# Kernel optimization log

Measured on AMD Instinct MI355X. Metric: run time of the kernel, lower is better.

Reference implementation:

```python
import jax, jax.numpy as jnp
import numpy as np


def _grid_sample_2d(plane, gx, gy):
    """Bilinear sample plane (C,H,W) at normalized coords gx,gy in [-1,1].
    align_corners=True convention (standard in tri-plane NeRF code).
    Returns (N, C)."""
    C, H, W = plane.shape
    ix = (gx + 1.0) * 0.5 * (W - 1)  # x indexes width
    iy = (gy + 1.0) * 0.5 * (H - 1)  # y indexes height
    x0f = jnp.floor(ix)
    y0f = jnp.floor(iy)
    wx = ix - x0f  # (N,)
    wy = iy - y0f
    x0 = jnp.clip(x0f.astype(jnp.int32), 0, W - 1)
    x1 = jnp.clip(x0 + 1, 0, W - 1)
    y0 = jnp.clip(y0f.astype(jnp.int32), 0, H - 1)
    y1 = jnp.clip(y0 + 1, 0, H - 1)
    flat = plane.reshape(C, H * W)

    def gather(yi, xi):  # -> (N, C)
        return jnp.take(flat, yi * W + xi, axis=1).T

    w00 = ((1 - wx) * (1 - wy))[:, None]
    w01 = (wx * (1 - wy))[:, None]
    w10 = ((1 - wx) * wy)[:, None]
    w11 = (wx * wy)[:, None]
    return (gather(y0, x0) * w00 + gather(y0, x1) * w01 +
            gather(y1, x0) * w10 + gather(y1, x1) * w11)


def setup_inputs() -> dict:
    key = jax.random.key(0)
    ks = jax.random.split(key, 7)
    N, C, H1, H2 = 2097152, 32, 256, 4
    res = (727, 314, 1300)
    pts = jax.random.uniform(ks[0], (N, 3), jnp.float32, minval=-1.0, maxval=1.0)
    s = 0.1  # small init like typical plane init
    plane_yx = jax.random.normal(ks[1], (C, res[1], res[0]), jnp.float32) * s
    plane_zx = jax.random.normal(ks[2], (C, res[2], res[0]), jnp.float32) * s
    plane_zy = jax.random.normal(ks[3], (C, res[2], res[1]), jnp.float32) * s
    w1 = jax.random.normal(ks[4], (C, H1), jnp.float32) * (1.0 / np.sqrt(C))
    b1 = jnp.zeros((H1,), jnp.float32)
    w2 = jax.random.normal(ks[5], (H1, H2), jnp.float32) * (1.0 / np.sqrt(H1))
    b2 = jnp.zeros((H2,), jnp.float32)
    return {"pts": pts, "plane_yx": plane_yx, "plane_zx": plane_zx,
            "plane_zy": plane_zy, "w1": w1, "b1": b1, "w2": w2, "b2": b2}


def reference(pts, plane_yx, plane_zx, plane_zy, w1, b1, w2, b2):
    # tri-plane feature fetch: pairs (x,y), (x,z), (y,z)
    f_yx = _grid_sample_2d(plane_yx, pts[:, 0], pts[:, 1])  # (N, C)
    f_zx = _grid_sample_2d(plane_zx, pts[:, 0], pts[:, 2])
    f_zy = _grid_sample_2d(plane_zy, pts[:, 1], pts[:, 2])
    features = f_yx * f_zx * f_zy  # elementwise product over planes
    h = jax.nn.relu(features @ w1 + b1)  # decoder MLP
    out = h @ w2 + b2  # (N, out_dim)
    return out
```

## Files before the change

kernel.cpp:

```cpp
#include <hip/hip_runtime.h>

#define NC    32
#define NH1   256
#define W_YX  727
#define H_YX  314
#define W_ZX  727
#define H_ZX  1300
#define W_ZY  314
#define H_ZY  1300
#define HW_YX (W_YX * H_YX)
#define HW_ZX (W_ZX * H_ZX)
#define HW_ZY (W_ZY * H_ZY)

#define FSTRIDE 17

typedef __attribute__((ext_vector_type(8))) short short8;
typedef __attribute__((ext_vector_type(4))) float f32x4;

__device__ __forceinline__ short f2bf(float f) {
    unsigned u = __float_as_uint(f);
    unsigned r = u + 0x7fffu + ((u >> 16) & 1u);
    return (short)(r >> 16);
}

__global__ __launch_bounds__(256) void kplane_transpose_bf16(
    const float* __restrict__ src, unsigned short* __restrict__ dst, int HW)
{
    __shared__ float tile[32][129];
    int hw0 = blockIdx.x * 128;
    int tx = threadIdx.x & 31, ty = threadIdx.x >> 5;
    if (hw0 + 128 <= HW) {
#pragma unroll
        for (int i = 0; i < 4; ++i) {
            int c = ty + i * 8;
            float4 v = *(const float4*)(src + (size_t)c * HW + hw0 + tx * 4);
            tile[c][tx * 4 + 0] = v.x; tile[c][tx * 4 + 1] = v.y;
            tile[c][tx * 4 + 2] = v.z; tile[c][tx * 4 + 3] = v.w;
        }
    } else {
        for (int i = 0; i < 4; ++i) {
            int c = ty + i * 8;
            for (int e = 0; e < 4; ++e) {
                int hw = hw0 + tx * 4 + e;
                tile[c][tx * 4 + e] = (hw < HW) ? src[(size_t)c * HW + hw] : 0.0f;
            }
        }
    }
    __syncthreads();
    int c8 = threadIdx.x & 3, r0 = threadIdx.x >> 2;
#pragma unroll
    for (int i = 0; i < 2; ++i) {
        int r = r0 + i * 64;
        int hw = hw0 + r;
        if (hw < HW) {
            uint4 o;
            unsigned* ou = (unsigned*)&o;
#pragma unroll
            for (int e = 0; e < 4; ++e) {
                unsigned lo = (unsigned)(unsigned short)f2bf(tile[c8 * 8 + 2 * e][r]);
                unsigned hi = (unsigned)(unsigned short)f2bf(tile[c8 * 8 + 2 * e + 1][r]);
                ou[e] = lo | (hi << 16);
            }
            *(uint4*)(dst + (size_t)hw * NC + c8 * 8) = o;
        }
    }
}

__global__ __launch_bounds__(256) void kplane_prep_w1(
    const float* __restrict__ w1, short* __restrict__ wb)
{
    int idx = blockIdx.x * 256 + threadIdx.x;
    int jj   = idx & 7;
    int lane = (idx >> 3) & 63;
    int nt   = idx >> 9;
    int n = nt * 16 + (lane & 15);
    int k = (lane >> 4) * 8 + jj;
    wb[idx] = f2bf(w1[k * NH1 + n]);
}

__device__ __forceinline__ void bilin2(
    float gx, float gy, int W, int H,
    unsigned& o0, unsigned& o1, float& wx, float& wy)
{
    float ix  = (gx + 1.0f) * 0.5f * (float)(W - 1);
    float iy  = (gy + 1.0f) * 0.5f * (float)(H - 1);
    float x0f = floorf(ix), y0f = floorf(iy);
    wx = ix - x0f; wy = iy - y0f;
    int x0 = (int)x0f; x0 = x0 < 0 ? 0 : (x0 > W - 1 ? W - 1 : x0);
    int y0 = (int)y0f; y0 = y0 < 0 ? 0 : (y0 > H - 1 ? H - 1 : y0);
    int y1 = y0 + 1; if (y1 > H - 1) y1 = H - 1;
    o0 = (unsigned)(y0 * W + x0) * 64u;
    o1 = (unsigned)(y1 * W + x0) * 64u;
}

__device__ __forceinline__ void sample8(
    const unsigned short* __restrict__ plane,
    unsigned o0, unsigned o1, float wy, float wxv, int j, float F[8])
{
    uint4 u0 = *(const uint4*)((const char*)plane + (size_t)o0 + j * 16);
    uint4 u1 = *(const uint4*)((const char*)plane + (size_t)o1 + j * 16);
    unsigned ua[4] = {u0.x, u0.y, u0.z, u0.w};
    unsigned ub[4] = {u1.x, u1.y, u1.z, u1.w};
#pragma unroll
    for (int e = 0; e < 4; ++e) {
        float a0 = __uint_as_float(ua[e] << 16);
        float a1 = __uint_as_float(ua[e] & 0xffff0000u);
        float b0 = __uint_as_float(ub[e] << 16);
        float b1 = __uint_as_float(ub[e] & 0xffff0000u);
        F[2 * e]     = wxv * fmaf(wy, b0 - a0, a0);
        F[2 * e + 1] = wxv * fmaf(wy, b1 - a1, a1);
    }
#pragma unroll
    for (int e = 0; e < 8; ++e)
        F[e] += __shfl_xor(F[e], 4, 64);
}

__global__ __launch_bounds__(256) void kplane_fused(
    const float* __restrict__ pts,
    const unsigned short* __restrict__ tyx,
    const unsigned short* __restrict__ tzx,
    const unsigned short* __restrict__ tzy,
    const short* __restrict__ w1b,
    const float* __restrict__ b1, const float* __restrict__ w2,
    const float* __restrict__ b2,
    float* __restrict__ out)
{
    __shared__ unsigned featS[256 * FSTRIDE];

    int t = threadIdx.x;
    int base = blockIdx.x * 256;
    int l = t & 63, j = t & 7;

    float px = pts[(size_t)(base + t) * 3 + 0];
    float py = pts[(size_t)(base + t) * 3 + 1];
    float pz = pts[(size_t)(base + t) * 3 + 2];
    unsigned ao0, ao1, co0, co1, do0, do1;
    float awx, awy, cwx, cwy, dwx, dwy;
    bilin2(px, py, W_YX, H_YX, ao0, ao1, awx, awy);
    bilin2(px, pz, W_ZX, H_ZX, co0, co1, cwx, cwy);
    bilin2(py, pz, W_ZY, H_ZY, do0, do1, dwx, dwy);

#pragma unroll
    for (int r = 0; r < 8; ++r) {
        int srcl = (l & 0x38) | r;
        int p = (t & ~7) | r;

        unsigned A0 = (unsigned)__shfl((int)ao0, srcl, 64);
        unsigned A1 = (unsigned)__shfl((int)ao1, srcl, 64);
        float AX = __shfl(awx, srcl, 64), AY = __shfl(awy, srcl, 64);
        unsigned C0 = (unsigned)__shfl((int)co0, srcl, 64);
        unsigned C1 = (unsigned)__shfl((int)co1, srcl, 64);
        float CX = __shfl(cwx, srcl, 64), CY = __shfl(cwy, srcl, 64);
        unsigned D0 = (unsigned)__shfl((int)do0, srcl, 64);
        unsigned D1 = (unsigned)__shfl((int)do1, srcl, 64);
        float DX = __shfl(dwx, srcl, 64), DY = __shfl(dwy, srcl, 64);

        float axv = (j & 4) ? AX : 1.0f - AX;
        float cxv = (j & 4) ? CX : 1.0f - CX;
        float dxv = (j & 4) ? DX : 1.0f - DX;

        float acc[8], tmp[8];
        sample8(tyx, A0, A1, AY, axv, j, acc);
        sample8(tzx, C0, C1, CY, cxv, j, tmp);
#pragma unroll
        for (int e = 0; e < 8; ++e) acc[e] *= tmp[e];
        sample8(tzy, D0, D1, DY, dxv, j, tmp);
#pragma unroll
        for (int e = 0; e < 8; ++e) acc[e] *= tmp[e];

        if (j < 4) {
#pragma unroll
            for (int e = 0; e < 4; ++e) {
                unsigned lo = (unsigned)(unsigned short)f2bf(acc[2 * e]);
                unsigned hi = (unsigned)(unsigned short)f2bf(acc[2 * e + 1]);
                featS[p * FSTRIDE + j * 4 + e] = lo | (hi << 16);
            }
        }
    }
    __syncthreads();

    {
        int w = t >> 6;
        int quad = l >> 4, l15 = l & 15;
        float4 b2v = *(const float4*)b2;
        const short8* Bw = (const short8*)w1b;

#pragma unroll
        for (int mt = 0; mt < 4; ++mt) {
            int p = w * 64 + mt * 16 + l15;
            union { unsigned u[4]; short8 s; } A;
#pragma unroll
            for (int e = 0; e < 4; ++e)
                A.u[e] = featS[p * FSTRIDE + quad * 4 + e];

            float4 oo0 = {0,0,0,0}, oo1 = {0,0,0,0}, oo2 = {0,0,0,0}, oo3 = {0,0,0,0};
#pragma unroll
            for (int nt = 0; nt < 16; ++nt) {
                short8 bh = Bw[nt * 64 + l];
                f32x4 z = {0.f, 0.f, 0.f, 0.f};
                z = __builtin_amdgcn_mfma_f32_16x16x32_bf16(A.s, bh, z, 0, 0, 0);
                float  b1v = b1[nt * 16 + l15];
                float4 w2v = ((const float4*)w2)[nt * 16 + l15];
                float h0 = fmaxf(z[0] + b1v, 0.f);
                float h1 = fmaxf(z[1] + b1v, 0.f);
                float h2 = fmaxf(z[2] + b1v, 0.f);
                float h3 = fmaxf(z[3] + b1v, 0.f);
                oo0.x = fmaf(h0, w2v.x, oo0.x); oo0.y = fmaf(h0, w2v.y, oo0.y);
                oo0.z = fmaf(h0, w2v.z, oo0.z); oo0.w = fmaf(h0, w2v.w, oo0.w);
                oo1.x = fmaf(h1, w2v.x, oo1.x); oo1.y = fmaf(h1, w2v.y, oo1.y);
                oo1.z = fmaf(h1, w2v.z, oo1.z); oo1.w = fmaf(h1, w2v.w, oo1.w);
                oo2.x = fmaf(h2, w2v.x, oo2.x); oo2.y = fmaf(h2, w2v.y, oo2.y);
                oo2.z = fmaf(h2, w2v.z, oo2.z); oo2.w = fmaf(h2, w2v.w, oo2.w);
                oo3.x = fmaf(h3, w2v.x, oo3.x); oo3.y = fmaf(h3, w2v.y, oo3.y);
                oo3.z = fmaf(h3, w2v.z, oo3.z); oo3.w = fmaf(h3, w2v.w, oo3.w);
            }
#pragma unroll
            for (int d = 1; d < 16; d <<= 1) {
                oo0.x += __shfl_xor(oo0.x, d); oo0.y += __shfl_xor(oo0.y, d);
                oo0.z += __shfl_xor(oo0.z, d); oo0.w += __shfl_xor(oo0.w, d);
                oo1.x += __shfl_xor(oo1.x, d); oo1.y += __shfl_xor(oo1.y, d);
                oo1.z += __shfl_xor(oo1.z, d); oo1.w += __shfl_xor(oo1.w, d);
                oo2.x += __shfl_xor(oo2.x, d); oo2.y += __shfl_xor(oo2.y, d);
                oo2.z += __shfl_xor(oo2.z, d); oo2.w += __shfl_xor(oo2.w, d);
                oo3.x += __shfl_xor(oo3.x, d); oo3.y += __shfl_xor(oo3.y, d);
                oo3.z += __shfl_xor(oo3.z, d); oo3.w += __shfl_xor(oo3.w, d);
            }
            if (l15 == 0) {
                int ptg = base + w * 64 + mt * 16 + quad * 4;
                float4* O = (float4*)out;
                float4 r0 = {oo0.x + b2v.x, oo0.y + b2v.y, oo0.z + b2v.z, oo0.w + b2v.w};
                float4 r1 = {oo1.x + b2v.x, oo1.y + b2v.y, oo1.z + b2v.z, oo1.w + b2v.w};
                float4 r2 = {oo2.x + b2v.x, oo2.y + b2v.y, oo2.z + b2v.z, oo2.w + b2v.w};
                float4 r3 = {oo3.x + b2v.x, oo3.y + b2v.y, oo3.z + b2v.z, oo3.w + b2v.w};
                O[ptg + 0] = r0; O[ptg + 1] = r1; O[ptg + 2] = r2; O[ptg + 3] = r3;
            }
        }
    }
}

__device__ __forceinline__ void bilin_full(
    float gx, float gy, int W, int H,
    int& o00, int& o01, int& o10, int& o11,
    float& w00, float& w01, float& w10, float& w11)
{
    float ix  = (gx + 1.0f) * 0.5f * (float)(W - 1);
    float iy  = (gy + 1.0f) * 0.5f * (float)(H - 1);
    float x0f = floorf(ix), y0f = floorf(iy);
    float wx  = ix - x0f,   wy  = iy - y0f;
    int x0 = (int)x0f; x0 = x0 < 0 ? 0 : (x0 > W - 1 ? W - 1 : x0);
    int y0 = (int)y0f; y0 = y0 < 0 ? 0 : (y0 > H - 1 ? H - 1 : y0);
    int x1 = x0 + 1; if (x1 > W - 1) x1 = W - 1;
    int y1 = y0 + 1; if (y1 > H - 1) y1 = H - 1;
    o00 = y0 * W + x0; o01 = y0 * W + x1;
    o10 = y1 * W + x0; o11 = y1 * W + x1;
    w00 = (1.0f - wx) * (1.0f - wy);
    w01 = wx * (1.0f - wy);
    w10 = (1.0f - wx) * wy;
    w11 = wx * wy;
}

__global__ __launch_bounds__(256) void kplane_fused_direct(
    const float* __restrict__ pts,
    const float* __restrict__ pyx, const float* __restrict__ pzx,
    const float* __restrict__ pzy,
    const float* __restrict__ w1, const float* __restrict__ b1,
    const float* __restrict__ w2, const float* __restrict__ b2,
    float* __restrict__ out, int N)
{
    int i = blockIdx.x * blockDim.x + threadIdx.x;
    if (i >= N) return;
    float px = pts[(size_t)i * 3 + 0];
    float py = pts[(size_t)i * 3 + 1];
    float pz = pts[(size_t)i * 3 + 2];

    int a00, a01, a10, a11; float aw00, aw01, aw10, aw11;
    int c00, c01, c10, c11; float cw00, cw01, cw10, cw11;
    int d00, d01, d10, d11; float dw00, dw01, dw10, dw11;
    bilin_full(px, py, W_YX, H_YX, a00, a01, a10, a11, aw00, aw01, aw10, aw11);
    bilin_full(px, pz, W_ZX, H_ZX, c00, c01, c10, c11, cw00, cw01, cw10, cw11);
    bilin_full(py, pz, W_ZY, H_ZY, d00, d01, d10, d11, dw00, dw01, dw10, dw11);

    float feat[NC];
#pragma unroll 4
    for (int c = 0; c < NC; ++c) {
        const float* byx = pyx + (size_t)c * HW_YX;
        const float* bzx = pzx + (size_t)c * HW_ZX;
        const float* bzy = pzy + (size_t)c * HW_ZY;
        float fyx = aw00 * byx[a00] + aw01 * byx[a01] + aw10 * byx[a10] + aw11 * byx[a11];
        float fzx = cw00 * bzx[c00] + cw01 * bzx[c01] + cw10 * bzx[c10] + cw11 * bzx[c11];
        float fzy = dw00 * bzy[d00] + dw01 * bzy[d01] + dw10 * bzy[d10] + dw11 * bzy[d11];
        feat[c] = fyx * fzx * fzy;
    }
    float o0 = b2[0], o1 = b2[1], o2 = b2[2], o3 = b2[3];
#pragma unroll 4
    for (int k = 0; k < NH1; ++k) {
        float hk = b1[k];
#pragma unroll
        for (int c = 0; c < NC; ++c)
            hk = fmaf(feat[c], w1[c * NH1 + k], hk);
        hk = fmaxf(hk, 0.0f);
        o0 = fmaf(hk, w2[k * 4 + 0], o0);
        o1 = fmaf(hk, w2[k * 4 + 1], o1);
        o2 = fmaf(hk, w2[k * 4 + 2], o2);
        o3 = fmaf(hk, w2[k * 4 + 3], o3);
    }
    float4 o; o.x = o0; o.y = o1; o.z = o2; o.w = o3;
    reinterpret_cast<float4*>(out)[i] = o;
}

extern "C" void kernel_launch(void* const* d_in, const int* in_sizes, int n_in,
                              void* d_out, int out_size, void* d_ws, size_t ws_size,
                              hipStream_t stream)
{
    const float* pts = (const float*)d_in[0];
    const float* pyx = (const float*)d_in[1];
    const float* pzx = (const float*)d_in[2];
    const float* pzy = (const float*)d_in[3];
    const float* w1  = (const float*)d_in[4];
    const float* b1  = (const float*)d_in[5];
    const float* w2  = (const float*)d_in[6];
    const float* b2  = (const float*)d_in[7];
    float* out = (float*)d_out;

    int N = in_sizes[0] / 3;

    size_t planes_e = (size_t)(HW_YX + HW_ZX + HW_ZY) * NC;
    size_t need = planes_e * sizeof(short) + 8192 * sizeof(short) + 256;

    if (ws_size >= need && (N % 256) == 0) {
        unsigned short* tyx = (unsigned short*)d_ws;
        unsigned short* tzx = tyx + (size_t)HW_YX * NC;
        unsigned short* tzy = tzx + (size_t)HW_ZX * NC;
        short* w1b = (short*)(tzy + (size_t)HW_ZY * NC);
        kplane_transpose_bf16<<<(HW_YX + 127) / 128, 256, 0, stream>>>(pyx, tyx, HW_YX);
        kplane_transpose_bf16<<<(HW_ZX + 127) / 128, 256, 0, stream>>>(pzx, tzx, HW_ZX);
        kplane_transpose_bf16<<<(HW_ZY + 127) / 128, 256, 0, stream>>>(pzy, tzy, HW_ZY);
        kplane_prep_w1<<<32, 256, 0, stream>>>(w1, w1b);
        kplane_fused<<<N / 256, 256, 0, stream>>>(pts, tyx, tzx, tzy,
                                                  w1b, b1, w2, b2, out);
    } else {
        int blocks = (N + 255) / 256;
        kplane_fused_direct<<<blocks, 256, 0, stream>>>(pts, pyx, pzx, pzy,
                                                        w1, b1, w2, b2, out, N);
    }
}
```

Before: 645.7 us.

## Move second MLP layer onto MFMA and restructure gather to four lanes per point

The second decoder layer, previously per-lane FMAs followed by a shuffle reduction, now runs as a bf16 MFMA. W1 is used as the A operand so the hidden activations come out already in the B-operand layout, and w2 is pre-packed with zero padding into that layout. The gather stage now stages per-point offsets and weights in shared memory and has four lanes per point each fetch 16-byte slices of all four corners, replacing the 8-lane shuffle and xor-reduce scheme. Hidden activations are rounded to bf16 before the second matmul, which adds precision loss, and the layer-2 MFMA pads its output dimension from 4 to 16.

```diff
diff --git a/kernel.cpp b/kernel.cpp
--- a/kernel.cpp
+++ b/kernel.cpp
@@ -1,4 +1,6 @@
 #include <hip/hip_runtime.h>
+#include <hip/hip_fp16.h>
+#include <hip/hip_bf16.h>
 
 #define NC    32
 #define NH1   256
@@ -12,7 +14,8 @@
 #define HW_ZX (W_ZX * H_ZX)
 #define HW_ZY (W_ZY * H_ZY)
 
-#define FSTRIDE 17
+#define PSTRIDE 12
+#define FSTRIDE 20
 
 typedef __attribute__((ext_vector_type(8))) short short8;
 typedef __attribute__((ext_vector_type(4))) float f32x4;
@@ -21,6 +24,11 @@
     unsigned u = __float_as_uint(f);
     unsigned r = u + 0x7fffu + ((u >> 16) & 1u);
     return (short)(r >> 16);
+}
+__device__ __forceinline__ unsigned pk2(float a, float b) {
+    union { __hip_bfloat162 h; unsigned u; } c;
+    c.h = __float22bfloat162_rn(make_float2(a, b));
+    return c.u;
 }
 
 __global__ __launch_bounds__(256) void kplane_transpose_bf16(
@@ -56,29 +64,40 @@
             uint4 o;
             unsigned* ou = (unsigned*)&o;
 #pragma unroll
-            for (int e = 0; e < 4; ++e) {
-                unsigned lo = (unsigned)(unsigned short)f2bf(tile[c8 * 8 + 2 * e][r]);
-                unsigned hi = (unsigned)(unsigned short)f2bf(tile[c8 * 8 + 2 * e + 1][r]);
-                ou[e] = lo | (hi << 16);
-            }
+            for (int e = 0; e < 4; ++e)
+                ou[e] = pk2(tile[c8 * 8 + 2 * e][r], tile[c8 * 8 + 2 * e + 1][r]);
             *(uint4*)(dst + (size_t)hw * NC + c8 * 8) = o;
         }
     }
 }
 
-__global__ __launch_bounds__(256) void kplane_prep_w1(
-    const float* __restrict__ w1, short* __restrict__ wb)
+__global__ __launch_bounds__(256) void kplane_prep_w1a(
+    const float* __restrict__ w1, short* __restrict__ w1a)
 {
     int idx = blockIdx.x * 256 + threadIdx.x;
-    int jj   = idx & 7;
+    int j    = idx & 7;
     int lane = (idx >> 3) & 63;
     int nt   = idx >> 9;
-    int n = nt * 16 + (lane & 15);
-    int k = (lane >> 4) * 8 + jj;
-    wb[idx] = f2bf(w1[k * NH1 + n]);
-}
-
-__device__ __forceinline__ void bilin2(
+    int ch  = (lane >> 4) * 8 + j;
+    int hid = nt * 16 + (lane & 15);
+    w1a[idx] = f2bf(w1[ch * NH1 + hid]);
+}
+
+__global__ __launch_bounds__(256) void kplane_prep_w2a(
+    const float* __restrict__ w2, short* __restrict__ w2a)
+{
+    int idx = blockIdx.x * 256 + threadIdx.x;
+    int j    = idx & 7;
+    int lane = (idx >> 3) & 63;
+    int kk   = idx >> 9;
+    int o    = lane & 15;
+    int quad = lane >> 4;
+    int hid  = (2 * kk + (j >> 2)) * 16 + quad * 4 + (j & 3);
+    float v  = (o < 4) ? w2[hid * 4 + o] : 0.0f;
+    w2a[idx] = f2bf(v);
+}
+
+__device__ __forceinline__ void bilin3(
     float gx, float gy, int W, int H,
     unsigned& o0, unsigned& o1, float& wx, float& wy)
 {
@@ -93,26 +112,34 @@
     o1 = (unsigned)(y1 * W + x0) * 64u;
 }
 
-__device__ __forceinline__ void sample8(
-    const unsigned short* __restrict__ plane,
-    unsigned o0, unsigned o1, float wy, float wxv, int j, float F[8])
-{
-    uint4 u0 = *(const uint4*)((const char*)plane + (size_t)o0 + j * 16);
-    uint4 u1 = *(const uint4*)((const char*)plane + (size_t)o1 + j * 16);
-    unsigned ua[4] = {u0.x, u0.y, u0.z, u0.w};
-    unsigned ub[4] = {u1.x, u1.y, u1.z, u1.w};
+template <bool FIRST>
+__device__ __forceinline__ void corner4(
+    const uint4& A, const uint4& B, const uint4& C, const uint4& D,
+    float wx, float wy, float F[8])
+{
+    float w00 = (1.0f - wx) * (1.0f - wy);
+    float w01 = wx * (1.0f - wy);
+    float w10 = (1.0f - wx) * wy;
+    float w11 = wx * wy;
+    const unsigned* ua = &A.x; const unsigned* ub = &B.x;
+    const unsigned* uc = &C.x; const unsigned* ud = &D.x;
 #pragma unroll
     for (int e = 0; e < 4; ++e) {
         float a0 = __uint_as_float(ua[e] << 16);
         float a1 = __uint_as_float(ua[e] & 0xffff0000u);
         float b0 = __uint_as_float(ub[e] << 16);
         float b1 = __uint_as_float(ub[e] & 0xffff0000u);
-        F[2 * e]     = wxv * fmaf(wy, b0 - a0, a0);
-        F[2 * e + 1] = wxv * fmaf(wy, b1 - a1, a1);
-    }
-#pragma unroll
-    for (int e = 0; e < 8; ++e)
-        F[e] += __shfl_xor(F[e], 4, 64);
+        float c0 = __uint_as_float(uc[e] << 16);
+        float c1 = __uint_as_float(uc[e] & 0xffff0000u);
+        float d0 = __uint_as_float(ud[e] << 16);
+        float d1 = __uint_as_float(ud[e] & 0xffff0000u);
+        float v0 = w00 * a0; v0 = fmaf(w01, b0, v0);
+        v0 = fmaf(w10, c0, v0); v0 = fmaf(w11, d0, v0);
+        float v1 = w00 * a1; v1 = fmaf(w01, b1, v1);
+        v1 = fmaf(w10, c1, v1); v1 = fmaf(w11, d1, v1);
+        if (FIRST) { F[2 * e] = v0; F[2 * e + 1] = v1; }
+        else       { F[2 * e] *= v0; F[2 * e + 1] *= v1; }
+    }
 }
 
 __global__ __launch_bounds__(256) void kplane_fused(
@@ -120,119 +147,111 @@
     const unsigned short* __restrict__ tyx,
     const unsigned short* __restrict__ tzx,
     const unsigned short* __restrict__ tzy,
-    const short* __restrict__ w1b,
-    const float* __restrict__ b1, const float* __restrict__ w2,
-    const float* __restrict__ b2,
+    const short* __restrict__ w1a, const short* __restrict__ w2a,
+    const float* __restrict__ b1, const float* __restrict__ b2,
     float* __restrict__ out)
 {
+    __shared__ unsigned parS[256 * PSTRIDE];
     __shared__ unsigned featS[256 * FSTRIDE];
 
     int t = threadIdx.x;
     int base = blockIdx.x * 256;
-    int l = t & 63, j = t & 7;
-
-    float px = pts[(size_t)(base + t) * 3 + 0];
-    float py = pts[(size_t)(base + t) * 3 + 1];
-    float pz = pts[(size_t)(base + t) * 3 + 2];
-    unsigned ao0, ao1, co0, co1, do0, do1;
-    float awx, awy, cwx, cwy, dwx, dwy;
-    bilin2(px, py, W_YX, H_YX, ao0, ao1, awx, awy);
-    bilin2(px, pz, W_ZX, H_ZX, co0, co1, cwx, cwy);
-    bilin2(py, pz, W_ZY, H_ZY, do0, do1, dwx, dwy);
-
-#pragma unroll
-    for (int r = 0; r < 8; ++r) {
-        int srcl = (l & 0x38) | r;
-        int p = (t & ~7) | r;
-
-        unsigned A0 = (unsigned)__shfl((int)ao0, srcl, 64);
-        unsigned A1 = (unsigned)__shfl((int)ao1, srcl, 64);
-        float AX = __shfl(awx, srcl, 64), AY = __shfl(awy, srcl, 64);
-        unsigned C0 = (unsigned)__shfl((int)co0, srcl, 64);
-        unsigned C1 = (unsigned)__shfl((int)co1, srcl, 64);
-        float CX = __shfl(cwx, srcl, 64), CY = __shfl(cwy, srcl, 64);
-        unsigned D0 = (unsigned)__shfl((int)do0, srcl, 64);
-        unsigned D1 = (unsigned)__shfl((int)do1, srcl, 64);
-        float DX = __shfl(dwx, srcl, 64), DY = __shfl(dwy, srcl, 64);
-
-        float axv = (j & 4) ? AX : 1.0f - AX;
-        float cxv = (j & 4) ? CX : 1.0f - CX;
-        float dxv = (j & 4) ? DX : 1.0f - DX;
-
-        float acc[8], tmp[8];
-        sample8(tyx, A0, A1, AY, axv, j, acc);
-        sample8(tzx, C0, C1, CY, cxv, j, tmp);
-#pragma unroll
-        for (int e = 0; e < 8; ++e) acc[e] *= tmp[e];
-        sample8(tzy, D0, D1, DY, dxv, j, tmp);
-#pragma unroll
-        for (int e = 0; e < 8; ++e) acc[e] *= tmp[e];
-
-        if (j < 4) {
-#pragma unroll
-            for (int e = 0; e < 4; ++e) {
-                unsigned lo = (unsigned)(unsigned short)f2bf(acc[2 * e]);
-                unsigned hi = (unsigned)(unsigned short)f2bf(acc[2 * e + 1]);
-                featS[p * FSTRIDE + j * 4 + e] = lo | (hi << 16);
+
+    {
+        float px = pts[(size_t)(base + t) * 3 + 0];
+        float py = pts[(size_t)(base + t) * 3 + 1];
+        float pz = pts[(size_t)(base + t) * 3 + 2];
+        unsigned a0, a1, c0, c1, d0, d1;
+        float awx, awy, cwx, cwy, dwx, dwy;
+        bilin3(px, py, W_YX, H_YX, a0, a1, awx, awy);
+        bilin3(px, pz, W_ZX, H_ZX, c0, c1, cwx, cwy);
+        bilin3(py, pz, W_ZY, H_ZY, d0, d1, dwx, dwy);
+        uint4* P = (uint4*)&parS[t * PSTRIDE];
+        uint4 P0 = {a0, a1, c0, c1};
+        uint4 P1 = {d0, d1, __float_as_uint(awx), __float_as_uint(awy)};
+        uint4 P2 = {__float_as_uint(cwx), __float_as_uint(cwy),
+                    __float_as_uint(dwx), __float_as_uint(dwy)};
+        P[0] = P0; P[1] = P1; P[2] = P2;
+    }
+    __syncthreads();
+
+    {
+        int q = t >> 2, j = t & 3;
+        int jx16 = j * 16;
+        const char* Byx = (const char*)tyx;
+        const char* Bzx = (const char*)tzx;
+        const char* Bzy = (const char*)tzy;
+#pragma unroll
+        for (int r = 0; r < 4; ++r) {
+            int p = r * 64 + q;
+            const uint4* P = (const uint4*)&parS[p * PSTRIDE];
+            uint4 P0 = P[0], P1 = P[1], P2 = P[2];
+            float awx = __uint_as_float(P1.z), awy = __uint_as_float(P1.w);
+            float cwx = __uint_as_float(P2.x), cwy = __uint_as_float(P2.y);
+            float dwx = __uint_as_float(P2.z), dwy = __uint_as_float(P2.w);
+
+            uint4 La = *(const uint4*)(Byx + P0.x + jx16);
+            uint4 Lb = *(const uint4*)(Byx + P0.x + 64 + jx16);
+            uint4 Lc = *(const uint4*)(Byx + P0.y + jx16);
+            uint4 Ld = *(const uint4*)(Byx + P0.y + 64 + jx16);
+            uint4 Ma = *(const uint4*)(Bzx + P0.z + jx16);
+            uint4 Mb = *(const uint4*)(Bzx + P0.z + 64 + jx16);
+            uint4 Mc = *(const uint4*)(Bzx + P0.w + jx16);
+            uint4 Md = *(const uint4*)(Bzx + P0.w + 64 + jx16);
+            uint4 Na = *(const uint4*)(Bzy + P1.x + jx16);
+            uint4 Nb = *(const uint4*)(Bzy + P1.x + 64 + jx16);
+            uint4 Nc = *(const uint4*)(Bzy + P1.y + jx16);
+            uint4 Nd = *(const uint4*)(Bzy + P1.y + 64 + jx16);
+
+            float F[8];
+            corner4<true >(La, Lb, Lc, Ld, awx, awy, F);
+            corner4<false>(Ma, Mb, Mc, Md, cwx, cwy, F);
+            corner4<false>(Na, Nb, Nc, Nd, dwx, dwy, F);
+
+            uint4 o;
+            o.x = pk2(F[0], F[1]); o.y = pk2(F[2], F[3]);
+            o.z = pk2(F[4], F[5]); o.w = pk2(F[6], F[7]);
+            *(uint4*)&featS[p * FSTRIDE + j * 4] = o;
+        }
+    }
+    __syncthreads();
+
+    {
+        int w = t >> 6, lane = t & 63;
+        int quad = lane >> 4, l15 = lane & 15;
+        const short8* W1A = (const short8*)w1a;
+        const short8* W2A = (const short8*)w2a;
+        const float4* B1v = (const float4*)b1;
+        float b20 = b2[0], b21 = b2[1], b22 = b2[2], b23 = b2[3];
+
+#pragma unroll
+        for (int mt = 0; mt < 4; ++mt) {
+            int pt = w * 64 + mt * 16 + l15;
+            union { uint4 v; short8 s; } bf;
+            bf.v = *(const uint4*)&featS[pt * FSTRIDE + quad * 4];
+
+            f32x4 acc = {0.f, 0.f, 0.f, 0.f};
+#pragma unroll
+            for (int kk = 0; kk < 8; ++kk) {
+                float4 be = B1v[(2 * kk) * 4 + quad];
+                float4 bo = B1v[(2 * kk + 1) * 4 + quad];
+                f32x4 ze = {be.x, be.y, be.z, be.w};
+                f32x4 zo = {bo.x, bo.y, bo.z, bo.w};
+                ze = __builtin_amdgcn_mfma_f32_16x16x32_bf16(
+                         W1A[(2 * kk) * 64 + lane], bf.s, ze, 0, 0, 0);
+                zo = __builtin_amdgcn_mfma_f32_16x16x32_bf16(
+                         W1A[(2 * kk + 1) * 64 + lane], bf.s, zo, 0, 0, 0);
+                union { unsigned u[4]; short8 s; } hb;
+                hb.u[0] = pk2(fmaxf(ze[0], 0.f), fmaxf(ze[1], 0.f));
+                hb.u[1] = pk2(fmaxf(ze[2], 0.f), fmaxf(ze[3], 0.f));
+                hb.u[2] = pk2(fmaxf(zo[0], 0.f), fmaxf(zo[1], 0.f));
+                hb.u[3] = pk2(fmaxf(zo[2], 0.f), fmaxf(zo[3], 0.f));
+                acc = __builtin_amdgcn_mfma_f32_16x16x32_bf16(
+                          W2A[kk * 64 + lane], hb.s, acc, 0, 0, 0);
             }
-        }
-    }
-    __syncthreads();
-
-    {
-        int w = t >> 6;
-        int quad = l >> 4, l15 = l & 15;
-        float4 b2v = *(const float4*)b2;
-        const short8* Bw = (const short8*)w1b;
-
-#pragma unroll
-        for (int mt = 0; mt < 4; ++mt) {
-            int p = w * 64 + mt * 16 + l15;
-            union { unsigned u[4]; short8 s; } A;
-#pragma unroll
-            for (int e = 0; e < 4; ++e)
-                A.u[e] = featS[p * FSTRIDE + quad * 4 + e];
-
-            float4 oo0 = {0,0,0,0}, oo1 = {0,0,0,0}, oo2 = {0,0,0,0}, oo3 = {0,0,0,0};
-#pragma unroll
-            for (int nt = 0; nt < 16; ++nt) {
-                short8 bh = Bw[nt * 64 + l];
-                f32x4 z = {0.f, 0.f, 0.f, 0.f};
-                z = __builtin_amdgcn_mfma_f32_16x16x32_bf16(A.s, bh, z, 0, 0, 0);
-                float  b1v = b1[nt * 16 + l15];
-                float4 w2v = ((const float4*)w2)[nt * 16 + l15];
-                float h0 = fmaxf(z[0] + b1v, 0.f);
-                float h1 = fmaxf(z[1] + b1v, 0.f);
-                float h2 = fmaxf(z[2] + b1v, 0.f);
-                float h3 = fmaxf(z[3] + b1v, 0.f);
-                oo0.x = fmaf(h0, w2v.x, oo0.x); oo0.y = fmaf(h0, w2v.y, oo0.y);
-                oo0.z = fmaf(h0, w2v.z, oo0.z); oo0.w = fmaf(h0, w2v.w, oo0.w);
-                oo1.x = fmaf(h1, w2v.x, oo1.x); oo1.y = fmaf(h1, w2v.y, oo1.y);
-                oo1.z = fmaf(h1, w2v.z, oo1.z); oo1.w = fmaf(h1, w2v.w, oo1.w);
-                oo2.x = fmaf(h2, w2v.x, oo2.x); oo2.y = fmaf(h2, w2v.y, oo2.y);
-                oo2.z = fmaf(h2, w2v.z, oo2.z); oo2.w = fmaf(h2, w2v.w, oo2.w);
-                oo3.x = fmaf(h3, w2v.x, oo3.x); oo3.y = fmaf(h3, w2v.y, oo3.y);
-                oo3.z = fmaf(h3, w2v.z, oo3.z); oo3.w = fmaf(h3, w2v.w, oo3.w);
-            }
-#pragma unroll
-            for (int d = 1; d < 16; d <<= 1) {
-                oo0.x += __shfl_xor(oo0.x, d); oo0.y += __shfl_xor(oo0.y, d);
-                oo0.z += __shfl_xor(oo0.z, d); oo0.w += __shfl_xor(oo0.w, d);
-                oo1.x += __shfl_xor(oo1.x, d); oo1.y += __shfl_xor(oo1.y, d);
-                oo1.z += __shfl_xor(oo1.z, d); oo1.w += __shfl_xor(oo1.w, d);
-                oo2.x += __shfl_xor(oo2.x, d); oo2.y += __shfl_xor(oo2.y, d);
-                oo2.z += __shfl_xor(oo2.z, d); oo2.w += __shfl_xor(oo2.w, d);
-                oo3.x += __shfl_xor(oo3.x, d); oo3.y += __shfl_xor(oo3.y, d);
-                oo3.z += __shfl_xor(oo3.z, d); oo3.w += __shfl_xor(oo3.w, d);
-            }
-            if (l15 == 0) {
-                int ptg = base + w * 64 + mt * 16 + quad * 4;
-                float4* O = (float4*)out;
-                float4 r0 = {oo0.x + b2v.x, oo0.y + b2v.y, oo0.z + b2v.z, oo0.w + b2v.w};
-                float4 r1 = {oo1.x + b2v.x, oo1.y + b2v.y, oo1.z + b2v.z, oo1.w + b2v.w};
-                float4 r2 = {oo2.x + b2v.x, oo2.y + b2v.y, oo2.z + b2v.z, oo2.w + b2v.w};
-                float4 r3 = {oo3.x + b2v.x, oo3.y + b2v.y, oo3.z + b2v.z, oo3.w + b2v.w};
-                O[ptg + 0] = r0; O[ptg + 1] = r1; O[ptg + 2] = r2; O[ptg + 3] = r3;
+            if (quad == 0) {
+                float4 o = {acc[0] + b20, acc[1] + b21, acc[2] + b22, acc[3] + b23};
+                ((float4*)out)[base + w * 64 + mt * 16 + l15] = o;
             }
         }
     }
@@ -325,19 +344,21 @@
     int N = in_sizes[0] / 3;
 
     size_t planes_e = (size_t)(HW_YX + HW_ZX + HW_ZY) * NC;
-    size_t need = planes_e * sizeof(short) + 8192 * sizeof(short) + 256;
+    size_t need = (planes_e + 8192 + 4096) * sizeof(short) + 256;
 
     if (ws_size >= need && (N % 256) == 0) {
         unsigned short* tyx = (unsigned short*)d_ws;
         unsigned short* tzx = tyx + (size_t)HW_YX * NC;
         unsigned short* tzy = tzx + (size_t)HW_ZX * NC;
-        short* w1b = (short*)(tzy + (size_t)HW_ZY * NC);
+        short* w1a = (short*)(tzy + (size_t)HW_ZY * NC);
+        short* w2a = w1a + 8192;
         kplane_transpose_bf16<<<(HW_YX + 127) / 128, 256, 0, stream>>>(pyx, tyx, HW_YX);
         kplane_transpose_bf16<<<(HW_ZX + 127) / 128, 256, 0, stream>>>(pzx, tzx, HW_ZX);
         kplane_transpose_bf16<<<(HW_ZY + 127) / 128, 256, 0, stream>>>(pzy, tzy, HW_ZY);
-        kplane_prep_w1<<<32, 256, 0, stream>>>(w1, w1b);
+        kplane_prep_w1a<<<32, 256, 0, stream>>>(w1, w1a);
+        kplane_prep_w2a<<<16, 256, 0, stream>>>(w2, w2a);
         kplane_fused<<<N / 256, 256, 0, stream>>>(pts, tyx, tzx, tzy,
-                                                  w1b, b1, w2, b2, out);
+                                                  w1a, w2a, b1, b2, out);
     } else {
         int blocks = (N + 255) / 256;
         kplane_fused_direct<<<blocks, 256, 0, stream>>>(pts, pyx, pzx, pzy,
```

New measurement: 602.0 us. 1.07x faster.
